# Performance work log

Hardware: AMD Instinct MI355X
Metric: run time of the kernel (lower is better)

## Reference

```python
import jax, jax.numpy as jnp
import numpy as np

# sRGB (D65) -> XYZ matrix and white point, as used by skimage.color.rgb2lab
_M = jnp.array([[0.412453, 0.357580, 0.180423],
                [0.212671, 0.715160, 0.072169],
                [0.019334, 0.119193, 0.950227]], dtype=jnp.float32)
_WHITE = jnp.array([0.95047, 1.0, 1.08883], dtype=jnp.float32)
_25POW7 = 25.0 ** 7


def _rgb2lab(rgb):
    # rgb: (..., 3) in [0,1]
    lin = jnp.where(rgb <= 0.04045, rgb / 12.92, ((rgb + 0.055) / 1.055) ** 2.4)
    xyz = jnp.einsum('...c,kc->...k', lin, _M) / _WHITE
    f = jnp.where(xyz > 0.008856, jnp.cbrt(xyz), 7.787 * xyz + 16.0 / 116.0)
    L = 116.0 * f[..., 1] - 16.0
    a = 500.0 * (f[..., 0] - f[..., 1])
    b = 200.0 * (f[..., 1] - f[..., 2])
    return L, a, b


def _ciede2000(L1, a1, b1, L2, a2, b2):
    C1 = jnp.hypot(a1, b1)
    C2 = jnp.hypot(a2, b2)
    Cbar = 0.5 * (C1 + C2)
    c7 = Cbar ** 7
    G = 0.5 * (1.0 - jnp.sqrt(c7 / (c7 + _25POW7)))
    a1p = a1 * (1.0 + G)
    a2p = a2 * (1.0 + G)
    C1p = jnp.hypot(a1p, b1)
    C2p = jnp.hypot(a2p, b2)
    h1 = jnp.rad2deg(jnp.arctan2(b1, a1p)) % 360.0
    h2 = jnp.rad2deg(jnp.arctan2(b2, a2p)) % 360.0

    dLp = L2 - L1
    dCp = C2p - C1p
    CC = C1p * C2p
    hdiff = h2 - h1
    dh = jnp.where(hdiff > 180.0, hdiff - 360.0,
                   jnp.where(hdiff < -180.0, hdiff + 360.0, hdiff))
    dh = jnp.where(CC == 0.0, 0.0, dh)
    dHp = 2.0 * jnp.sqrt(CC) * jnp.sin(0.5 * jnp.deg2rad(dh))

    Lbar = 0.5 * (L1 + L2)
    Cbarp = 0.5 * (C1p + C2p)
    hsum = h1 + h2
    hbar = jnp.where(jnp.abs(h1 - h2) <= 180.0, 0.5 * hsum,
                     jnp.where(hsum < 360.0, 0.5 * (hsum + 360.0), 0.5 * (hsum - 360.0)))
    hbar = jnp.where(CC == 0.0, hsum, hbar)
    hr = jnp.deg2rad(hbar)
    T = (1.0 - 0.17 * jnp.cos(hr - jnp.deg2rad(30.0))
         + 0.24 * jnp.cos(2.0 * hr)
         + 0.32 * jnp.cos(3.0 * hr + jnp.deg2rad(6.0))
         - 0.20 * jnp.cos(4.0 * hr - jnp.deg2rad(63.0)))

    Lm50sq = (Lbar - 50.0) ** 2
    Sl = 1.0 + 0.015 * Lm50sq / jnp.sqrt(20.0 + Lm50sq)
    Sc = 1.0 + 0.045 * Cbarp
    Sh = 1.0 + 0.015 * Cbarp * T
    dtheta = 30.0 * jnp.exp(-(((hbar - 275.0) / 25.0) ** 2))
    cb7 = Cbarp ** 7
    Rc = 2.0 * jnp.sqrt(cb7 / (cb7 + _25POW7))
    Rt = -Rc * jnp.sin(2.0 * jnp.deg2rad(dtheta))

    tL = dLp / Sl
    tC = dCp / Sc
    tH = dHp / Sh
    return jnp.sqrt(jnp.maximum(tL * tL + tC * tC + tH * tH + Rt * tC * tH, 0.0))


def setup_inputs() -> dict:
    key = jax.random.key(0)
    k1, k2 = jax.random.split(key)
    B, C, H, W = 32, 3, 512, 512
    genImage = jax.random.uniform(k1, (B, C, H, W), dtype=jnp.float32)
    gtImage = jax.random.uniform(k2, (B, C, H, W), dtype=jnp.float32)
    return {"genImage": genImage, "gtImage": gtImage}


def reference(genImage, gtImage) -> jnp.ndarray:
    B, C, H, W = genImage.shape
    # Faithful to original torchTensorToNumpy: a plain reshape (3,H,W)->(H,W,3),
    # NOT a transpose. Batched: (B,3,H,W)->(B,H,W,3) by reshape.
    gen = genImage.reshape(B, H, W, 3)
    gt = gtImage.reshape(B, H, W, 3)
    L1, a1, b1 = _rgb2lab(gt)
    L2, a2, b2 = _rgb2lab(gen)
    dE = jnp.abs(_ciede2000(L1, a1, b1, L2, a2, b2))
    # normalize=None in __init__, so no /255. mean over pixels then over batch
    # equals overall mean for equal-size images.
    return jnp.mean(dE)
```

## Files before the change

### kernel.cpp

```cpp
#include <hip/hip_runtime.h>


__device__ __forceinline__ float fexp2(float x) { return __builtin_amdgcn_exp2f(x); }
__device__ __forceinline__ float flog2(float x) { return __builtin_amdgcn_logf(x); }
__device__ __forceinline__ float frcp(float x)  { return __builtin_amdgcn_rcpf(x); }
__device__ __forceinline__ float fsqrt_(float x){ return __builtin_amdgcn_sqrtf(x); }
__device__ __forceinline__ float frsq(float x)  { return __builtin_amdgcn_rsqf(x); }
__device__ __forceinline__ float ffract(float x){ return __builtin_amdgcn_fractf(x); }
__device__ __forceinline__ float sin_rev(float x) { return __builtin_amdgcn_sinf(ffract(x)); }

__device__ __forceinline__ float pow7f(float x) {
    float x2 = x * x;
    float x3 = x2 * x;
    return x3 * x3 * x;
}

__device__ __forceinline__ float atan2_rev(float y, float x) {
    float ax = fabsf(x), ay = fabsf(y);
    float mx = fmaxf(ax, ay), mn = fminf(ax, ay);
    float a = mn * frcp(mx);
    if (mx == 0.0f) a = 0.0f;
    float s = a * a;
    float p = fmaf(s, fmaf(s, fmaf(s, fmaf(s, fmaf(s,
              -1.1721200e-2f, 5.2653320e-2f), -1.1643287e-1f),
               1.9354346e-1f), -3.3262347e-1f), 9.9997726e-1f);
    float r = a * p * 0.15915494309189535f;
    if (ay > ax) r = 0.25f - r;
    if (x < 0.0f) r = 0.5f - r;
    if (y < 0.0f) r = -r;
    return r;
}

__device__ __forceinline__ float srgb_lin(float v) {
    float p = fexp2(2.4f * flog2((v + 0.055f) * (1.0f / 1.055f)));
    return (v <= 0.04045f) ? v * (1.0f / 12.92f) : p;
}

__device__ __forceinline__ float fxyz(float t) {
    float c = fexp2(0.3333333333333333f * flog2(t));
    return (t > 0.008856f) ? c : fmaf(7.787f, t, 16.0f / 116.0f);
}

__device__ __forceinline__ void rgb2lab(float r, float g, float b,
                                        float& L, float& A, float& B) {
    float rl = srgb_lin(r), gl = srgb_lin(g), bl = srgb_lin(b);
    float x = fmaf(0.43395296f, rl, fmaf(0.37621626f, gl, 0.18982646f * bl));
    float y = fmaf(0.212671f,  rl, fmaf(0.715160f,  gl, 0.072169f  * bl));
    float z = fmaf(0.017757f,  rl, fmaf(0.10946953f, gl, 0.87271810f * bl));
    float fx = fxyz(x), fy = fxyz(y), fz = fxyz(z);
    L = fmaf(116.0f, fy, -16.0f);
    A = 500.0f * (fx - fy);
    B = 200.0f * (fy - fz);
}

__device__ __forceinline__ float ciede2000(float L1, float a1, float b1,
                                           float L2, float a2, float b2) {
    const float P25_7 = 6103515625.0f;

    float b1sq = b1 * b1, b2sq = b2 * b2;
    float C1 = fsqrt_(fmaf(a1, a1, b1sq));
    float C2 = fsqrt_(fmaf(a2, a2, b2sq));
    float Cbar = 0.5f * (C1 + C2);
    float c7 = pow7f(Cbar);
    float G1 = 1.5f - 0.5f * fsqrt_(c7 * frcp(c7 + P25_7));
    float a1p = a1 * G1;
    float a2p = a2 * G1;
    float C1p = fsqrt_(fmaf(a1p, a1p, b1sq));
    float C2p = fsqrt_(fmaf(a2p, a2p, b2sq));
    float CC  = C1p * C2p;

    float dot   = fmaf(a1p, a2p, b1 * b2);
    float cross = fmaf(b2, a1p, -a2p * b1);
    float dHp = copysignf(fsqrt_(fmaxf(2.0f * (CC - dot), 0.0f)), cross);

    float dLp = L2 - L1;
    float dCp = C2p - C1p;

    float sx = fmaf(a1p, C2p, a2p * C1p);
    float sy = fmaf(b1,  C2p, b2  * C1p);
    float n2 = fmaf(sx, sx, sy * sy);
    float inv = (n2 > 0.0f) ? frsq(n2) : 0.0f;
    float ch = sx * inv, sh = sy * inv;

    float c2 = fmaf(2.0f * ch, ch, -1.0f);
    float s2 = 2.0f * sh * ch;
    float c3 = fmaf(c2, ch, -s2 * sh);
    float s3 = fmaf(s2, ch,  c2 * sh);
    float c4 = fmaf(2.0f * c2, c2, -1.0f);
    float s4 = 2.0f * s2 * c2;
    float T = 1.0f
            - 0.17f * fmaf(ch, 0.8660254037844387f, sh * 0.5f)
            + 0.24f * c2
            + 0.32f * fmaf(c3, 0.9945218953682733f, -s3 * 0.10452846326765347f)
            - 0.20f * fmaf(c4, 0.45399049973954675f, s4 * 0.8910065241883679f);

    float hbar = atan2_rev(sy, sx);
    if (hbar < 0.0f) hbar += 1.0f;

    float Lbar  = 0.5f * (L1 + L2);
    float Cbarp = 0.5f * (C1p + C2p);
    float Lm50 = Lbar - 50.0f;
    float q = Lm50 * Lm50;
    float Sl = fmaf(0.015f * q, frsq(20.0f + q), 1.0f);
    float Sc = fmaf(0.045f, Cbarp, 1.0f);
    float Sh = fmaf(0.015f * Cbarp, T, 1.0f);

    float td = fmaf(hbar, 14.4f, -11.0f);
    float dtheta = 30.0f * fexp2(-1.4426950408889634f * td * td);
    float cb7 = pow7f(Cbarp);
    float Rc = 2.0f * fsqrt_(cb7 * frcp(cb7 + P25_7));
    float Rt = -Rc * sin_rev(dtheta * (1.0f / 180.0f));

    float ScSh = Sc * Sh;
    float R3 = frcp(Sl * ScSh);
    float tL = dLp * ScSh * R3;
    float tC = dCp * (Sl * Sh) * R3;
    float tH = dHp * (Sl * Sc) * R3;
    float s = fmaf(tL, tL, fmaf(tC, tC, fmaf(tH, tH, Rt * tC * tH)));
    return fsqrt_(fmaxf(s, 0.0f));
}

__device__ __forceinline__ float de_px(float gr, float gg, float gb,
                                       float rr, float rg, float rb) {
    float L1, A1, B1, L2, A2, B2;
    rgb2lab(rr, rg, rb, L1, A1, B1);
    rgb2lab(gr, gg, gb, L2, A2, B2);
    return fabsf(ciede2000(L1, A1, B1, L2, A2, B2));
}

__device__ __forceinline__ void process4(const float4& g0, const float4& g1,
                                         const float4& g2, const float4& r0,
                                         const float4& r1, const float4& r2,
                                         float& acc) {
    acc += de_px(g0.x, g0.y, g0.z, r0.x, r0.y, r0.z);
    acc += de_px(g0.w, g1.x, g1.y, r0.w, r1.x, r1.y);
    acc += de_px(g1.z, g1.w, g2.x, r1.z, r1.w, r2.x);
    acc += de_px(g2.y, g2.z, g2.w, r2.y, r2.z, r2.w);
}

__device__ __forceinline__ void block_reduce_store(float acc, float* dst) {
    for (int off = 32; off > 0; off >>= 1) acc += __shfl_down(acc, off, 64);
    __shared__ float sm[4];
    int lane = threadIdx.x & 63;
    int wid  = threadIdx.x >> 6;
    if (lane == 0) sm[wid] = acc;
    __syncthreads();
    if (threadIdx.x == 0) *dst = sm[0] + sm[1] + sm[2] + sm[3];
}

template <int NITER>
__global__ __launch_bounds__(256, 4) void de_main_fix(const float4* __restrict__ gen,
                                                      const float4* __restrict__ gt,
                                                      float* __restrict__ partial,
                                                      int stride) {
    int t = blockIdx.x * 256 + threadIdx.x;
    float acc = 0.0f;

    float4 cg0 = gen[3 * t + 0], cg1 = gen[3 * t + 1], cg2 = gen[3 * t + 2];
    float4 cr0 = gt [3 * t + 0], cr1 = gt [3 * t + 1], cr2 = gt [3 * t + 2];

    #pragma unroll 1
    for (int it = 0; it < NITER - 1; ++it) {
        int tn = t + stride;
        float4 ng0 = gen[3 * tn + 0], ng1 = gen[3 * tn + 1], ng2 = gen[3 * tn + 2];
        float4 nr0 = gt [3 * tn + 0], nr1 = gt [3 * tn + 1], nr2 = gt [3 * tn + 2];
        __builtin_amdgcn_sched_barrier(0);
        process4(cg0, cg1, cg2, cr0, cr1, cr2, acc);
        cg0 = ng0; cg1 = ng1; cg2 = ng2;
        cr0 = nr0; cr1 = nr1; cr2 = nr2;
        t = tn;
    }
    process4(cg0, cg1, cg2, cr0, cr1, cr2, acc);

    block_reduce_store(acc, &partial[blockIdx.x]);
}

__global__ __launch_bounds__(256, 4) void de_main_gen(const float4* __restrict__ gen,
                                                      const float4* __restrict__ gt,
                                                      float* __restrict__ partial,
                                                      int ntrip) {
    int tid = blockIdx.x * blockDim.x + threadIdx.x;
    int stride = gridDim.x * blockDim.x;
    float acc = 0.0f;
    for (int t = tid; t < ntrip; t += stride) {
        float4 g0 = gen[3 * t + 0], g1 = gen[3 * t + 1], g2 = gen[3 * t + 2];
        float4 r0 = gt [3 * t + 0], r1 = gt [3 * t + 1], r2 = gt [3 * t + 2];
        process4(g0, g1, g2, r0, r1, r2, acc);
    }
    block_reduce_store(acc, &partial[blockIdx.x]);
}

__global__ __launch_bounds__(256) void de_final(const float* __restrict__ partial,
                                                float* __restrict__ out,
                                                int n, float inv_npix) {
    float acc = 0.0f;
    for (int i = threadIdx.x; i < n; i += 256) acc += partial[i];
    for (int off = 32; off > 0; off >>= 1) acc += __shfl_down(acc, off, 64);
    __shared__ float sm[4];
    int lane = threadIdx.x & 63;
    int wid  = threadIdx.x >> 6;
    if (lane == 0) sm[wid] = acc;
    __syncthreads();
    if (threadIdx.x == 0) out[0] = (sm[0] + sm[1] + sm[2] + sm[3]) * inv_npix;
}

extern "C" void kernel_launch(void* const* d_in, const int* in_sizes, int n_in,
                              void* d_out, int out_size, void* d_ws, size_t ws_size,
                              hipStream_t stream) {
    const float4* gen = (const float4*)d_in[0];
    const float4* gt  = (const float4*)d_in[1];

    const int total_f = in_sizes[0];
    const int ntrip   = total_f / 12;
    const int npix    = total_f / 3;

    float* partial = (float*)d_ws;
    const int blocks  = 2048;
    const int threads = blocks * 256;

    if (ntrip == threads * 4) {
        de_main_fix<4><<<blocks, 256, 0, stream>>>(gen, gt, partial, threads);
    } else {
        de_main_gen<<<blocks, 256, 0, stream>>>(gen, gt, partial, ntrip);
    }
    de_final<<<1, 256, 0, stream>>>(partial, (float*)d_out,
                                    blocks, 1.0f / (float)npix);
}
```

Baseline: 71.65 us.

## Replace hue atan2 with angular-distance series, polynomial sin, one-shot grid

Computes the hue-rotation term from the cosine of the angle between the mean-hue unit vector and 275 degrees, using a half-angle arcsine series instead of a full atan2 polynomial. Replaces the hardware sin with a short Taylor polynomial for sin(2*dtheta). Also drops the software-pipelined 4-iteration loop in favour of an 8192-block grid where each thread handles one float4 triple, with no occupancy hint in launch bounds. This trims ALU work and register pressure per pixel, at the cost of approximation accuracy near large angles and more blocks and partials to reduce.

```diff
diff --git a/kernel.cpp b/kernel.cpp
--- a/kernel.cpp
+++ b/kernel.cpp
@@ -6,29 +6,11 @@
 __device__ __forceinline__ float frcp(float x)  { return __builtin_amdgcn_rcpf(x); }
 __device__ __forceinline__ float fsqrt_(float x){ return __builtin_amdgcn_sqrtf(x); }
 __device__ __forceinline__ float frsq(float x)  { return __builtin_amdgcn_rsqf(x); }
-__device__ __forceinline__ float ffract(float x){ return __builtin_amdgcn_fractf(x); }
-__device__ __forceinline__ float sin_rev(float x) { return __builtin_amdgcn_sinf(ffract(x)); }
 
 __device__ __forceinline__ float pow7f(float x) {
     float x2 = x * x;
     float x3 = x2 * x;
     return x3 * x3 * x;
-}
-
-__device__ __forceinline__ float atan2_rev(float y, float x) {
-    float ax = fabsf(x), ay = fabsf(y);
-    float mx = fmaxf(ax, ay), mn = fminf(ax, ay);
-    float a = mn * frcp(mx);
-    if (mx == 0.0f) a = 0.0f;
-    float s = a * a;
-    float p = fmaf(s, fmaf(s, fmaf(s, fmaf(s, fmaf(s,
-              -1.1721200e-2f, 5.2653320e-2f), -1.1643287e-1f),
-               1.9354346e-1f), -3.3262347e-1f), 9.9997726e-1f);
-    float r = a * p * 0.15915494309189535f;
-    if (ay > ax) r = 0.25f - r;
-    if (x < 0.0f) r = 0.5f - r;
-    if (y < 0.0f) r = -r;
-    return r;
 }
 
 __device__ __forceinline__ float srgb_lin(float v) {
@@ -94,8 +76,15 @@
             + 0.32f * fmaf(c3, 0.9945218953682733f, -s3 * 0.10452846326765347f)
             - 0.20f * fmaf(c4, 0.45399049973954675f, s4 * 0.8910065241883679f);
 
-    float hbar = atan2_rev(sy, sx);
-    if (hbar < 0.0f) hbar += 1.0f;
+    const float C275 = 0.08715574f;
+    const float S275 = -0.9961947f;
+    float cphi = fmaf(ch, C275, sh * S275);
+    float u2 = fmaf(-0.5f, cphi, 0.5f);
+    float u  = fsqrt_(fmaxf(u2, 0.0f));
+    float halfphi = u * fmaf(u2, fmaf(u2, fmaf(u2, 0.044642857f, 0.075f),
+                                      0.16666667f), 1.0f);
+    float td = halfphi * 4.5836624f;
+    float dtheta = 30.0f * fexp2(-1.4426950408889634f * td * td);
 
     float Lbar  = 0.5f * (L1 + L2);
     float Cbarp = 0.5f * (C1p + C2p);
@@ -105,11 +94,12 @@
     float Sc = fmaf(0.045f, Cbarp, 1.0f);
     float Sh = fmaf(0.015f * Cbarp, T, 1.0f);
 
-    float td = fmaf(hbar, 14.4f, -11.0f);
-    float dtheta = 30.0f * fexp2(-1.4426950408889634f * td * td);
     float cb7 = pow7f(Cbarp);
     float Rc = 2.0f * fsqrt_(cb7 * frcp(cb7 + P25_7));
-    float Rt = -Rc * sin_rev(dtheta * (1.0f / 180.0f));
+    float xr = dtheta * 0.034906585f;
+    float xr2 = xr * xr;
+    float sin2dt = xr * fmaf(xr2, fmaf(xr2, 8.3333338e-3f, -1.6666667e-1f), 1.0f);
+    float Rt = -Rc * sin2dt;
 
     float ScSh = Sc * Sh;
     float R3 = frcp(Sl * ScSh);
@@ -128,14 +118,15 @@
     return fabsf(ciede2000(L1, A1, B1, L2, A2, B2));
 }
 
-__device__ __forceinline__ void process4(const float4& g0, const float4& g1,
-                                         const float4& g2, const float4& r0,
-                                         const float4& r1, const float4& r2,
-                                         float& acc) {
-    acc += de_px(g0.x, g0.y, g0.z, r0.x, r0.y, r0.z);
+__device__ __forceinline__ float process4(const float4& g0, const float4& g1,
+                                          const float4& g2, const float4& r0,
+                                          const float4& r1, const float4& r2) {
+    float acc;
+    acc  = de_px(g0.x, g0.y, g0.z, r0.x, r0.y, r0.z);
     acc += de_px(g0.w, g1.x, g1.y, r0.w, r1.x, r1.y);
     acc += de_px(g1.z, g1.w, g2.x, r1.z, r1.w, r2.x);
     acc += de_px(g2.y, g2.z, g2.w, r2.y, r2.z, r2.w);
+    return acc;
 }
 
 __device__ __forceinline__ void block_reduce_store(float acc, float* dst) {
@@ -148,44 +139,27 @@
     if (threadIdx.x == 0) *dst = sm[0] + sm[1] + sm[2] + sm[3];
 }
 
-template <int NITER>
-__global__ __launch_bounds__(256, 4) void de_main_fix(const float4* __restrict__ gen,
-                                                      const float4* __restrict__ gt,
-                                                      float* __restrict__ partial,
-                                                      int stride) {
+__global__ __launch_bounds__(256) void de_main1(const float4* __restrict__ gen,
+                                                const float4* __restrict__ gt,
+                                                float* __restrict__ partial) {
     int t = blockIdx.x * 256 + threadIdx.x;
-    float acc = 0.0f;
-
-    float4 cg0 = gen[3 * t + 0], cg1 = gen[3 * t + 1], cg2 = gen[3 * t + 2];
-    float4 cr0 = gt [3 * t + 0], cr1 = gt [3 * t + 1], cr2 = gt [3 * t + 2];
-
-    #pragma unroll 1
-    for (int it = 0; it < NITER - 1; ++it) {
-        int tn = t + stride;
-        float4 ng0 = gen[3 * tn + 0], ng1 = gen[3 * tn + 1], ng2 = gen[3 * tn + 2];
-        float4 nr0 = gt [3 * tn + 0], nr1 = gt [3 * tn + 1], nr2 = gt [3 * tn + 2];
-        __builtin_amdgcn_sched_barrier(0);
-        process4(cg0, cg1, cg2, cr0, cr1, cr2, acc);
-        cg0 = ng0; cg1 = ng1; cg2 = ng2;
-        cr0 = nr0; cr1 = nr1; cr2 = nr2;
-        t = tn;
-    }
-    process4(cg0, cg1, cg2, cr0, cr1, cr2, acc);
-
+    float4 g0 = gen[3 * t + 0], g1 = gen[3 * t + 1], g2 = gen[3 * t + 2];
+    float4 r0 = gt [3 * t + 0], r1 = gt [3 * t + 1], r2 = gt [3 * t + 2];
+    float acc = process4(g0, g1, g2, r0, r1, r2);
     block_reduce_store(acc, &partial[blockIdx.x]);
 }
 
-__global__ __launch_bounds__(256, 4) void de_main_gen(const float4* __restrict__ gen,
-                                                      const float4* __restrict__ gt,
-                                                      float* __restrict__ partial,
-                                                      int ntrip) {
+__global__ __launch_bounds__(256) void de_main_gen(const float4* __restrict__ gen,
+                                                   const float4* __restrict__ gt,
+                                                   float* __restrict__ partial,
+                                                   int ntrip) {
     int tid = blockIdx.x * blockDim.x + threadIdx.x;
     int stride = gridDim.x * blockDim.x;
     float acc = 0.0f;
     for (int t = tid; t < ntrip; t += stride) {
         float4 g0 = gen[3 * t + 0], g1 = gen[3 * t + 1], g2 = gen[3 * t + 2];
         float4 r0 = gt [3 * t + 0], r1 = gt [3 * t + 1], r2 = gt [3 * t + 2];
-        process4(g0, g1, g2, r0, r1, r2, acc);
+        acc += process4(g0, g1, g2, r0, r1, r2);
     }
     block_reduce_store(acc, &partial[blockIdx.x]);
 }
@@ -215,14 +189,15 @@
     const int npix    = total_f / 3;
 
     float* partial = (float*)d_ws;
-    const int blocks  = 2048;
-    const int threads = blocks * 256;
-
-    if (ntrip == threads * 4) {
-        de_main_fix<4><<<blocks, 256, 0, stream>>>(gen, gt, partial, threads);
+
+    if (ntrip == 8192 * 256) {
+        de_main1<<<8192, 256, 0, stream>>>(gen, gt, partial);
+        de_final<<<1, 256, 0, stream>>>(partial, (float*)d_out,
+                                        8192, 1.0f / (float)npix);
     } else {
+        const int blocks = 2048;
         de_main_gen<<<blocks, 256, 0, stream>>>(gen, gt, partial, ntrip);
+        de_final<<<1, 256, 0, stream>>>(partial, (float*)d_out,
+                                        blocks, 1.0f / (float)npix);
     }
-    de_final<<<1, 256, 0, stream>>>(partial, (float*)d_out,
-                                    blocks, 1.0f / (float)npix);
-}
+}
```

After: 77.24 us. 1.08x slower.
